# Kernel tuning notes

Hardware: AMD Instinct MI355X
Metric: run time of the kernel (lower is better)

Reference implementation:

```python
import jax, jax.numpy as jnp
import numpy as np

B_SZ, SEQ, CH, ORDER = 8, 8192, 256, 64
EPS_LN = 1e-5
EPS_H = 1e-6


def setup_inputs() -> dict:
    key = jax.random.key(0)
    ks = jax.random.split(key, 12)
    s = 1.0 / np.sqrt(CH)
    x = jax.random.normal(ks[0], (B_SZ, SEQ, CH), jnp.float32)
    # RTF params: A = denominator coeffs (monic, leading 1 implied), B = numerator coeffs
    A = 0.01 * jax.random.normal(ks[1], (CH, ORDER), jnp.float32)  # small -> stable 1/A(z)
    Bp = 0.1 * jax.random.normal(ks[2], (CH, ORDER), jnp.float32)
    h0 = jnp.zeros((1,), jnp.float32)  # init torch.tensor([0.])
    W_enc = s * jax.random.normal(ks[3], (CH, CH), jnp.float32)
    b_enc = jnp.zeros((CH,), jnp.float32)
    W_fc = s * jax.random.normal(ks[4], (CH, CH), jnp.float32)
    b_fc = jnp.zeros((CH,), jnp.float32)
    gamma = jnp.ones((CH,), jnp.float32)
    beta = jnp.zeros((CH,), jnp.float32)
    W_dec = s * jax.random.normal(ks[5], (CH, CH), jnp.float32)
    b_dec = jnp.zeros((CH,), jnp.float32)
    return {"x": x, "A": A, "Bp": Bp, "h0": h0, "W_enc": W_enc, "b_enc": b_enc,
            "W_fc": W_fc, "b_fc": b_fc, "gamma": gamma, "beta": beta,
            "W_dec": W_dec, "b_dec": b_dec}


def _rtf_kernel(A, Bp, L):
    # K(z) = B(z)/A(z) with monic denominator a = [1, A_1..A_order]
    C = A.shape[0]
    a = jnp.concatenate([jnp.ones((C, 1), A.dtype), A], axis=1)  # (C, order+1)
    af = jnp.fft.rfft(a, n=L, axis=1)
    bf = jnp.fft.rfft(Bp, n=L, axis=1)
    return jnp.fft.irfft(bf / af, n=L, axis=1)  # (C, L)


def _causal_fft_conv(x, K):
    # x: (B, L, C); K: (C, L) per-channel causal filter
    L = x.shape[1]
    n = 2 * L
    xf = jnp.fft.rfft(x, n=n, axis=1)            # (B, n/2+1, C)
    Kf = jnp.fft.rfft(K.T, n=n, axis=0)          # (n/2+1, C)
    return jnp.fft.irfft(xf * Kf[None], n=n, axis=1)[:, :L]


def reference(x, A, Bp, h0, W_enc, b_enc, W_fc, b_fc, gamma, beta, W_dec, b_dec):
    gelu = lambda t: jax.nn.gelu(t, approximate=False)
    xe = x @ W_enc.T + b_enc                      # encode
    L = xe.shape[1]
    K = _rtf_kernel(A, Bp, L)                     # kernel generation from (A,B)
    h1 = _causal_fft_conv(xe, K)                  # FFT long convolution
    y1 = gelu(h1 + h0 * xe)                       # SSMRTF output (mult_activation=gelu)
    y2 = gelu(y1 @ W_fc.T + b_fc)                 # fc + final_act
    y2 = y2 + xe                                  # skip
    mu = jnp.mean(y2, axis=-1, keepdims=True)     # LayerNorm over channels
    var = jnp.mean(jnp.square(y2 - mu), axis=-1, keepdims=True)
    y2 = (y2 - mu) * jax.lax.rsqrt(var + EPS_LN) * gamma + beta
    y = y2 @ W_dec.T + b_dec                      # decode
    # h = ||y||_inf over seq / ||x_enc||_inf over seq
    h = jnp.max(jnp.abs(y), axis=1) / (jnp.max(jnp.abs(xe), axis=1) + EPS_H)
    return (y, h)
```

## Files before the change

kernel.cpp:

```cpp
#include <hip/hip_runtime.h>
#include <math.h>


#define BSZ   8
#define SEQ   8192
#define CHN   256
#define ORD   64
#define STAPS 512
#define NDD   17
#define PREPAD 544
#define XROW  (PREPAD + SEQ)
#define MTOT  (BSZ * SEQ)
#define YELEMS (MTOT * CHN)

#define CT     2048
#define CROWE  3072

typedef short s16x8 __attribute__((ext_vector_type(8)));
typedef float f32x4 __attribute__((ext_vector_type(4)));

#define MFMA16(a, b, c) __builtin_amdgcn_mfma_f32_16x16x32_bf16((a), (b), (c), 0, 0, 0)

__device__ __forceinline__ void gll16(const void* g, void* l) {
  __builtin_amdgcn_global_load_lds(
      (const __attribute__((address_space(1))) unsigned int*)g,
      (__attribute__((address_space(3))) unsigned int*)l, 16, 0, 0);
}

#define PERMC(row, h) (((row) * 8 + ((h) ^ ((row) & 7))) * 8)

__device__ __forceinline__ unsigned short f2bf(float f) {
  unsigned u = __float_as_uint(f);
  return (unsigned short)((u + 0x7FFFu + ((u >> 16) & 1u)) >> 16);
}
__device__ __forceinline__ float bf2f(unsigned short h) {
  return __uint_as_float(((unsigned)h) << 16);
}
__device__ __forceinline__ float geluf(float x) {
  float x2 = x * x;
  float y = x * __builtin_fmaf(0.0356774081f, x2, 0.7978845608f);
  float e = __builtin_amdgcn_exp2f(-2.8853900818f * y);
  return x * __builtin_amdgcn_rcpf(1.0f + e);
}
__device__ __forceinline__ uint4 packbf8(float4 a, float4 b) {
  uint4 r;
  r.x = (unsigned)f2bf(a.x) | ((unsigned)f2bf(a.y) << 16);
  r.y = (unsigned)f2bf(a.z) | ((unsigned)f2bf(a.w) << 16);
  r.z = (unsigned)f2bf(b.x) | ((unsigned)f2bf(b.y) << 16);
  r.w = (unsigned)f2bf(b.z) | ((unsigned)f2bf(b.w) << 16);
  return r;
}

__global__ __launch_bounds__(256) void k_prep(const float* we, const float* wf,
                                              const float* wd, unsigned short* owe,
                                              unsigned short* owf, unsigned short* owd) {
  int i = blockIdx.x * 256 + threadIdx.x;
  int which = i >> 16, off = i & 65535;
  if (which == 0)      owe[off] = f2bf(we[off]);
  else if (which == 1) owf[off] = f2bf(wf[off]);
  else                 owd[off] = f2bf(wd[off]);
}

__global__ __launch_bounds__(256) void k_zero(unsigned short* xeT, uint4* maxbufs) {
  int i = blockIdx.x * 256 + threadIdx.x;
  uint4 z; z.x = 0; z.y = 0; z.z = 0; z.w = 0;
  if (i < 2048 * 68) {
    int row = i / 68, cc = i % 68;
    *(uint4*)((char*)xeT + (size_t)row * (XROW * 2) + (size_t)cc * 16) = z;
  } else {
    int j = i - 2048 * 68;
    if (j < 1024) maxbufs[j] = z;
  }
}

__global__ __launch_bounds__(256) void k_kgen(const float* A, const float* Bp,
                                              unsigned short* afr) {
  __shared__ float Gs[4][STAPS];
  __shared__ float Et[4][64];
  __shared__ float Ac[4][65];
  __shared__ float Bb[4][64];
  __shared__ float Kb[4][STAPS];
  int lane = threadIdx.x & 63, wv = threadIdx.x >> 6;
  int c = blockIdx.x * 4 + wv;
  Ac[wv][lane + 1] = A[(size_t)c * ORD + lane];
  Bb[wv][lane]     = Bp[(size_t)c * ORD + lane];
  if (lane == 0) { Ac[wv][0] = 1.f; Gs[wv][0] = 1.f; }
  __syncthreads();

  for (int n = 1; n < STAPS; n <<= 1) {
    float e = 0.f;
    int uhi = min(n + lane, 64);
    for (int u = lane + 1; u <= uhi; ++u)
      e += Ac[wv][u] * Gs[wv][n + lane - u];
    Et[wv][lane] = e;
    __syncthreads();
    int nk = (n + 63) >> 6;
    for (int k = 0; k < nk; ++k) {
      int idx = k * 64 + lane;
      if (idx < n) {
        float acc = 0.f;
        int imax = min(idx, 63);
        for (int i = 0; i <= imax; ++i)
          acc += Et[wv][i] * Gs[wv][idx - i];
        Gs[wv][n + idx] = -acc;
      }
    }
    __syncthreads();
  }

  for (int k = 0; k < 8; ++k) {
    int t = k * 64 + lane;
    float acc = 0.f;
    int jmax = min(t, 63);
    for (int j = 0; j <= jmax; ++j)
      acc += Bb[wv][j] * Gs[wv][t - j];
    Kb[wv][t] = acc;
  }
  __syncthreads();

  int m = lane & 15, quad = lane >> 4;
  for (int dd = 0; dd < NDD; ++dd) {
    unsigned short v[8];
#pragma unroll
    for (int j = 0; j < 8; ++j) {
      int k = quad * 8 + j;
      int d = 2 * dd + (k >> 4);
      int p = k & 15;
      int s = 16 * d + m - p;
      float kv = (s >= 0 && s < STAPS) ? Kb[wv][s] : 0.f;
      v[j] = f2bf(kv);
    }
    uint4 pk;
    pk.x = (unsigned)v[0] | ((unsigned)v[1] << 16);
    pk.y = (unsigned)v[2] | ((unsigned)v[3] << 16);
    pk.z = (unsigned)v[4] | ((unsigned)v[5] << 16);
    pk.w = (unsigned)v[6] | ((unsigned)v[7] << 16);
    *(uint4*)(afr + ((size_t)(c * NDD + dd) * 64 + lane) * 8) = pk;
  }
}

__global__ __launch_bounds__(256) void k_gemm1(const float* x, const unsigned short* wb,
                                               const float* benc, unsigned short* xeT,
                                               unsigned int* maxxe) {
  __shared__ __align__(16) unsigned short As[256 * 64];
  __shared__ __align__(16) unsigned short Bs[64 * 64];
  int tid = threadIdx.x, lane = tid & 63, wv = tid >> 6;
  int ln15 = lane & 15, hf = lane >> 4;
  size_t t0 = (size_t)blockIdx.x * 64;
  int b = (int)(t0 >> 13), tin = (int)(t0 & 8191);
  f32x4 acc[4][4];
#pragma unroll
  for (int i = 0; i < 4; ++i)
#pragma unroll
    for (int j = 0; j < 4; ++j) { acc[i][j][0]=0.f; acc[i][j][1]=0.f; acc[i][j][2]=0.f; acc[i][j][3]=0.f; }

  for (int k0 = 0; k0 < CHN; k0 += 64) {
    __syncthreads();
#pragma unroll
    for (int i = 0; i < 8; ++i) {
      int p = 512 * wv + 64 * i + lane;
      int row = p >> 3, h = (p & 7) ^ (row & 7);
      gll16(wb + (size_t)row * CHN + k0 + h * 8, &As[(512 * wv + 64 * i) * 8]);
    }
    {
      int row = tid >> 2, hb = (tid & 3) * 2;
      const float* src = x + (t0 + row) * CHN + k0 + hb * 8;
      float4 f0 = *(const float4*)src;
      float4 f1 = *(const float4*)(src + 4);
      float4 f2 = *(const float4*)(src + 8);
      float4 f3 = *(const float4*)(src + 12);
      *(uint4*)&Bs[PERMC(row, hb)]     = packbf8(f0, f1);
      *(uint4*)&Bs[PERMC(row, hb + 1)] = packbf8(f2, f3);
    }
    __syncthreads();
#pragma unroll
    for (int ks = 0; ks < 2; ++ks) {
      s16x8 af[4], bfr[4];
#pragma unroll
      for (int mt = 0; mt < 4; ++mt) {
        int row = 64 * wv + 16 * mt + ln15;
        af[mt] = *(const s16x8*)&As[PERMC(row, ks * 4 + hf)];
      }
#pragma unroll
      for (int nt = 0; nt < 4; ++nt) {
        int row = 16 * nt + ln15;
        bfr[nt] = *(const s16x8*)&Bs[PERMC(row, ks * 4 + hf)];
      }
#pragma unroll
      for (int mt = 0; mt < 4; ++mt)
#pragma unroll
        for (int nt = 0; nt < 4; ++nt)
          acc[mt][nt] = MFMA16(af[mt], bfr[nt], acc[mt][nt]);
    }
  }
  int quad = hf;
#pragma unroll
  for (int mt = 0; mt < 4; ++mt) {
#pragma unroll
    for (int r = 0; r < 4; ++r) {
      int row = 64 * wv + 16 * mt + 4 * quad + r;
      float bias = benc[row];
      float mv = 0.f;
#pragma unroll
      for (int nt = 0; nt < 4; ++nt) {
        float v = acc[mt][nt][r] + bias;
        int t = tin + 16 * nt + ln15;
        xeT[(size_t)(b * CHN + row) * XROW + PREPAD + t] = f2bf(v);
        mv = fmaxf(mv, fabsf(v));
      }
      mv = fmaxf(mv, __shfl_xor(mv, 1)); mv = fmaxf(mv, __shfl_xor(mv, 2));
      mv = fmaxf(mv, __shfl_xor(mv, 4)); mv = fmaxf(mv, __shfl_xor(mv, 8));
      if (ln15 == 0) atomicMax(&maxxe[b * CHN + row], __float_as_uint(mv));
    }
  }
}

__global__ __launch_bounds__(256) void k_conv(const unsigned short* xeT,
                                              const unsigned short* afr,
                                              unsigned short* y1, const float* h0p) {
  __shared__ __align__(16) unsigned short xet[4 * CROWE];
  __shared__ __align__(16) unsigned short bnc[4 * CT];
  int tid = threadIdx.x, lane = tid & 63, wv = tid >> 6;
  int idx = blockIdx.x;
  int tg = idx & 3, cg = (idx >> 2) & 63, b = idx >> 8;
  int c0 = cg * 4, t0 = tg * CT;
  int c = c0 + wv;

  s16x8 afrg[NDD];
  {
    const unsigned short* ap = afr + (size_t)c * (NDD * 512) + (size_t)lane * 8;
#pragma unroll
    for (int dd = 0; dd < NDD; ++dd)
      afrg[dd] = *(const s16x8*)(ap + (size_t)dd * 512);
  }
  {
    int lp = lane ^ ((lane >> 3) & 7);
    const unsigned short* gbase = xeT + (size_t)(b * CHN + c) * XROW + t0;
    unsigned short* lbase = &xet[wv * CROWE];
#pragma unroll
    for (int k = 0; k < 6; ++k)
      gll16(gbase + (size_t)(64 * k + lp) * 8, &lbase[k * 64 * 8]);
  }
  float h0 = h0p[0];

  int n = lane & 15, quad = lane >> 4;
  int qc = quad - ((quad >> 1) << 2);
  const char* xb = (const char*)&xet[wv * CROWE];

  int ad[NDD];
  {
    int cb0 = 2 * n + qc + 68;
#pragma unroll
    for (int dd = 0; dd < NDD; ++dd) {
      int cc = cb0 - 4 * dd;
      ad[dd] = (cc ^ ((cc >> 3) & 7)) * 16;
    }
  }
  int ead;
  {
    int ch = 68 + 2 * n + (quad >> 1);
    ead = (ch ^ ((ch >> 3) & 7)) * 16 + 8 * (quad & 1);
  }
  __syncthreads();

#pragma unroll 1
  for (int s = 0; s < 8; ++s) {
    f32x4 a0, a1;
    a0[0]=0.f; a0[1]=0.f; a0[2]=0.f; a0[3]=0.f;
    a1[0]=0.f; a1[1]=0.f; a1[2]=0.f; a1[3]=0.f;
#pragma unroll
    for (int dd = 0; dd < 16; dd += 2) {
      a0 = MFMA16(afrg[dd],     *(const s16x8*)(xb + ad[dd]),     a0);
      a1 = MFMA16(afrg[dd + 1], *(const s16x8*)(xb + ad[dd + 1]), a1);
    }
    a0 = MFMA16(afrg[16], *(const s16x8*)(xb + ad[16]), a0);
    uint2 xvp = *(const uint2*)(xb + ead);
    unsigned short o[4];
#pragma unroll
    for (int r = 0; r < 4; ++r) {
      float xv = bf2f(((const unsigned short*)&xvp)[r]);
      float v = (a0[r] + a1[r]) + h0 * xv;
      o[r] = f2bf(geluf(v));
    }
    uint2 pw;
    pw.x = (unsigned)o[0] | ((unsigned)o[1] << 16);
    pw.y = (unsigned)o[2] | ((unsigned)o[3] << 16);
    *(uint2*)&bnc[wv * CT + 256 * s + 16 * n + 4 * quad] = pw;
#pragma unroll
    for (int dd = 16; dd >= 8; --dd) ad[dd] = ad[dd - 8];
#pragma unroll
    for (int dd = 0; dd < 8; ++dd) ad[dd] = (ad[dd] + 512) ^ 64;
    ead = (ead + 512) ^ 64;
  }
  __syncthreads();
  {
    const size_t obase = (size_t)(b * SEQ + t0) * CHN + c0;
#pragma unroll
    for (int s = 0; s < 8; ++s) {
      int tl = 256 * s + tid;
      uint2 pk;
      pk.x = (unsigned)bnc[tl] | ((unsigned)bnc[CT + tl] << 16);
      pk.y = (unsigned)bnc[2 * CT + tl] | ((unsigned)bnc[3 * CT + tl] << 16);
      *(uint2*)(y1 + obase + (size_t)tl * CHN) = pk;
    }
  }
}

__global__ __launch_bounds__(256) void k_gemm2(const unsigned short* y1,
                                               const unsigned short* wb, const float* bfc,
                                               const unsigned short* xeT, const float* gam,
                                               const float* bet, unsigned short* y2n) {
  __shared__ __align__(16) unsigned short Ws[256 * 64];
  __shared__ __align__(16) unsigned short Asb[64 * 64];
  __shared__ float pl[64][2][2];
  int tid = threadIdx.x, lane = tid & 63, wv = tid >> 6;
  int ln15 = lane & 15, hf = lane >> 4, quad = hf;
  size_t M0 = (size_t)blockIdx.x * 64;
  int b = (int)(M0 >> 13), tin = (int)(M0 & 8191);
  int mh = wv & 1, nh = wv >> 1;
  f32x4 acc[2][8];
#pragma unroll
  for (int i = 0; i < 2; ++i)
#pragma unroll
    for (int j = 0; j < 8; ++j) { acc[i][j][0]=0.f; acc[i][j][1]=0.f; acc[i][j][2]=0.f; acc[i][j][3]=0.f; }

  for (int k0 = 0; k0 < CHN; k0 += 64) {
    __syncthreads();
#pragma unroll
    for (int i = 0; i < 8; ++i) {
      int p = 512 * wv + 64 * i + lane;
      int row = p >> 3, h = (p & 7) ^ (row & 7);
      gll16(wb + (size_t)row * CHN + k0 + h * 8, &Ws[(512 * wv + 64 * i) * 8]);
    }
#pragma unroll
    for (int i = 0; i < 2; ++i) {
      int p = 128 * wv + 64 * i + lane;
      int row = p >> 3, h = (p & 7) ^ (row & 7);
      gll16(y1 + (M0 + row) * CHN + k0 + h * 8, &Asb[(128 * wv + 64 * i) * 8]);
    }
    __syncthreads();
#pragma unroll
    for (int ks = 0; ks < 2; ++ks) {
      s16x8 af[2], bfr[8];
#pragma unroll
      for (int mt = 0; mt < 2; ++mt) {
        int row = 32 * mh + 16 * mt + ln15;
        af[mt] = *(const s16x8*)&Asb[PERMC(row, ks * 4 + hf)];
      }
#pragma unroll
      for (int nt = 0; nt < 8; ++nt) {
        int row = 128 * nh + 16 * nt + ln15;
        bfr[nt] = *(const s16x8*)&Ws[PERMC(row, ks * 4 + hf)];
      }
#pragma unroll
      for (int mt = 0; mt < 2; ++mt)
#pragma unroll
        for (int nt = 0; nt < 8; ++nt)
          acc[mt][nt] = MFMA16(af[mt], bfr[nt], acc[mt][nt]);
    }
  }
  float g8[8], be8[8], bf8[8];
#pragma unroll
  for (int nt = 0; nt < 8; ++nt) {
    int col = 128 * nh + 16 * nt + ln15;
    g8[nt] = gam[col]; be8[nt] = bet[col]; bf8[nt] = bfc[col];
  }
#pragma unroll
  for (int mt = 0; mt < 2; ++mt) {
    int mlb = 32 * mh + 16 * mt + 4 * quad;
    uint2 xv2[8];
#pragma unroll
    for (int nt = 0; nt < 8; ++nt) {
      int col = 128 * nh + 16 * nt + ln15;
      xv2[nt] = *(const uint2*)(xeT + (size_t)(b * CHN + col) * XROW + PREPAD + tin + mlb);
    }
#pragma unroll
    for (int r = 0; r < 4; ++r) {
      int ml = mlb + r;
      float s1 = 0.f, s2 = 0.f;
#pragma unroll
      for (int nt = 0; nt < 8; ++nt) {
        float t2 = acc[mt][nt][r] + bf8[nt];
        float xv = bf2f(((const unsigned short*)&xv2[nt])[r]);
        float y2 = geluf(t2) + xv;
        acc[mt][nt][r] = y2;
        s1 += y2; s2 += y2 * y2;
      }
      s1 += __shfl_xor(s1, 1); s2 += __shfl_xor(s2, 1);
      s1 += __shfl_xor(s1, 2); s2 += __shfl_xor(s2, 2);
      s1 += __shfl_xor(s1, 4); s2 += __shfl_xor(s2, 4);
      s1 += __shfl_xor(s1, 8); s2 += __shfl_xor(s2, 8);
      if (ln15 == 0) { pl[ml][nh][0] = s1; pl[ml][nh][1] = s2; }
    }
  }
  __syncthreads();
#pragma unroll
  for (int mt = 0; mt < 2; ++mt) {
#pragma unroll
    for (int r = 0; r < 4; ++r) {
      int ml = 32 * mh + 16 * mt + 4 * quad + r;
      float s1 = pl[ml][0][0] + pl[ml][1][0];
      float s2 = pl[ml][0][1] + pl[ml][1][1];
      float mu = s1 * (1.f / 256.f);
      float var = s2 * (1.f / 256.f) - mu * mu;
      float ri = rsqrtf(var + 1e-5f);
#pragma unroll
      for (int nt = 0; nt < 8; ++nt) {
        int col = 128 * nh + 16 * nt + ln15;
        float yn = (acc[mt][nt][r] - mu) * ri * g8[nt] + be8[nt];
        y2n[(M0 + ml) * CHN + col] = f2bf(yn);
      }
    }
  }
}

__global__ __launch_bounds__(256) void k_gemm3(const unsigned short* y2n,
                                               const unsigned short* wb, const float* bd,
                                               float* yout, unsigned int* maxy) {
  __shared__ __align__(16) unsigned short Ws[256 * 64];
  __shared__ __align__(16) unsigned short Asb[64 * 64];
  int tid = threadIdx.x, lane = tid & 63, wv = tid >> 6;
  int ln15 = lane & 15, hf = lane >> 4, quad = hf;
  size_t M0 = (size_t)blockIdx.x * 64;
  int b = (int)(M0 >> 13);
  int mh = wv & 1, nh = wv >> 1;
  f32x4 acc[2][8];
#pragma unroll
  for (int i = 0; i < 2; ++i)
#pragma unroll
    for (int j = 0; j < 8; ++j) { acc[i][j][0]=0.f; acc[i][j][1]=0.f; acc[i][j][2]=0.f; acc[i][j][3]=0.f; }

  for (int k0 = 0; k0 < CHN; k0 += 64) {
    __syncthreads();
#pragma unroll
    for (int i = 0; i < 8; ++i) {
      int p = 512 * wv + 64 * i + lane;
      int row = p >> 3, h = (p & 7) ^ (row & 7);
      gll16(wb + (size_t)row * CHN + k0 + h * 8, &Ws[(512 * wv + 64 * i) * 8]);
    }
#pragma unroll
    for (int i = 0; i < 2; ++i) {
      int p = 128 * wv + 64 * i + lane;
      int row = p >> 3, h = (p & 7) ^ (row & 7);
      gll16(y2n + (M0 + row) * CHN + k0 + h * 8, &Asb[(128 * wv + 64 * i) * 8]);
    }
    __syncthreads();
#pragma unroll
    for (int ks = 0; ks < 2; ++ks) {
      s16x8 af[2], bfr[8];
#pragma unroll
      for (int mt = 0; mt < 2; ++mt) {
        int row = 32 * mh + 16 * mt + ln15;
        af[mt] = *(const s16x8*)&Asb[PERMC(row, ks * 4 + hf)];
      }
#pragma unroll
      for (int nt = 0; nt < 8; ++nt) {
        int row = 128 * nh + 16 * nt + ln15;
        bfr[nt] = *(const s16x8*)&Ws[PERMC(row, ks * 4 + hf)];
      }
#pragma unroll
      for (int mt = 0; mt < 2; ++mt)
#pragma unroll
        for (int nt = 0; nt < 8; ++nt)
          acc[mt][nt] = MFMA16(af[mt], bfr[nt], acc[mt][nt]);
    }
  }
  float bd8[8];
#pragma unroll
  for (int nt = 0; nt < 8; ++nt) bd8[nt] = bd[128 * nh + 16 * nt + ln15];
#pragma unroll
  for (int mt = 0; mt < 2; ++mt)
#pragma unroll
    for (int r = 0; r < 4; ++r) {
      int ml = 32 * mh + 16 * mt + 4 * quad + r;
#pragma unroll
      for (int nt = 0; nt < 8; ++nt) {
        int col = 128 * nh + 16 * nt + ln15;
        float v = acc[mt][nt][r] + bd8[nt];
        acc[mt][nt][r] = v;
        yout[(M0 + ml) * CHN + col] = v;
      }
    }
#pragma unroll
  for (int nt = 0; nt < 8; ++nt) {
    int col = 128 * nh + 16 * nt + ln15;
    float mv = 0.f;
#pragma unroll
    for (int mt = 0; mt < 2; ++mt)
#pragma unroll
      for (int r = 0; r < 4; ++r) mv = fmaxf(mv, fabsf(acc[mt][nt][r]));
    mv = fmaxf(mv, __shfl_xor(mv, 16));
    mv = fmaxf(mv, __shfl_xor(mv, 32));
    if (quad == 0) atomicMax(&maxy[b * CHN + col], __float_as_uint(mv));
  }
}

__global__ __launch_bounds__(256) void k_hfin(const unsigned int* maxxe,
                                              const unsigned int* maxy, float* hout) {
  int i = blockIdx.x * 256 + threadIdx.x;
  if (i < BSZ * CHN) {
    float mx = __uint_as_float(maxxe[i]);
    float my = __uint_as_float(maxy[i]);
    hout[i] = my / (mx + 1e-6f);
  }
}

extern "C" void kernel_launch(void* const* d_in, const int* in_sizes, int n_in,
                              void* d_out, int out_size, void* d_ws, size_t ws_size,
                              hipStream_t stream) {
  const float* x   = (const float*)d_in[0];
  const float* A   = (const float*)d_in[1];
  const float* Bp  = (const float*)d_in[2];
  const float* h0  = (const float*)d_in[3];
  const float* We  = (const float*)d_in[4];
  const float* be  = (const float*)d_in[5];
  const float* Wf  = (const float*)d_in[6];
  const float* bfc = (const float*)d_in[7];
  const float* gam = (const float*)d_in[8];
  const float* bet = (const float*)d_in[9];
  const float* Wd  = (const float*)d_in[10];
  const float* bd  = (const float*)d_in[11];

  char* ws = (char*)d_ws;
  unsigned short* y1  = (unsigned short*)(ws + 0);
  unsigned short* afr = (unsigned short*)(ws + 33554432);
  unsigned short* web = (unsigned short*)(ws + 38010880);
  unsigned short* wfb = (unsigned short*)(ws + 38141952);
  unsigned short* wdb = (unsigned short*)(ws + 38273024);
  unsigned int*  maxxe = (unsigned int*)(ws + 38404096);
  unsigned int*  maxy  = (unsigned int*)(ws + 38412288);

  unsigned short* xeT = (unsigned short*)d_out;
  float* yout = (float*)d_out;
  float* hout = yout + YELEMS;

  k_prep<<<768, 256, 0, stream>>>(We, Wf, Wd, web, wfb, wdb);
  k_zero<<<548, 256, 0, stream>>>(xeT, (uint4*)maxxe);
  k_kgen<<<64, 256, 0, stream>>>(A, Bp, afr);
  k_gemm1<<<1024, 256, 0, stream>>>(x, web, be, xeT, maxxe);
  k_conv<<<2048, 256, 0, stream>>>(xeT, afr, y1, h0);
  k_gemm2<<<1024, 256, 0, stream>>>(y1, wfb, bfc, xeT, gam, bet, y1);
  k_gemm3<<<1024, 256, 0, stream>>>(y1, wdb, bd, yout, maxy);
  k_hfin<<<8, 256, 0, stream>>>(maxxe, maxy, hout);
}
```

Baseline: 296.8 us.

## Merge prep/zero kernels and fold kernel generation into first GEMM launch

Combines weight conversion and buffer zeroing into one launch, and runs the RTF kernel-generation work as 64 extra blocks inside the encoder GEMM launch so the two overlap. The kgen code now keeps the A coefficients in registers and uses fully unrolled fixed-length loops over a zero-padded shared buffer, replacing the variable-bound loops. This removes two launch boundaries and the serial latency of the small kgen kernel, at the cost of more registers and shared memory in the combined GEMM kernel, which may lower its occupancy.

Measured after the change: 279.6 us. -5.8%, faster.

```diff
diff --git a/kernel.cpp b/kernel.cpp
--- a/kernel.cpp
+++ b/kernel.cpp
@@ -51,59 +51,66 @@
   return r;
 }
 
-__global__ __launch_bounds__(256) void k_prep(const float* we, const float* wf,
-                                              const float* wd, unsigned short* owe,
-                                              unsigned short* owf, unsigned short* owd) {
-  int i = blockIdx.x * 256 + threadIdx.x;
-  int which = i >> 16, off = i & 65535;
-  if (which == 0)      owe[off] = f2bf(we[off]);
-  else if (which == 1) owf[off] = f2bf(wf[off]);
-  else                 owd[off] = f2bf(wd[off]);
-}
-
-__global__ __launch_bounds__(256) void k_zero(unsigned short* xeT, uint4* maxbufs) {
-  int i = blockIdx.x * 256 + threadIdx.x;
-  uint4 z; z.x = 0; z.y = 0; z.z = 0; z.w = 0;
-  if (i < 2048 * 68) {
-    int row = i / 68, cc = i % 68;
-    *(uint4*)((char*)xeT + (size_t)row * (XROW * 2) + (size_t)cc * 16) = z;
+__global__ __launch_bounds__(256) void k_pz(const float* we, const float* wf,
+                                            const float* wd, unsigned short* owe,
+                                            unsigned short* owf, unsigned short* owd,
+                                            unsigned short* xeT, uint4* maxbufs) {
+  int bx = blockIdx.x, tid = threadIdx.x;
+  if (bx < 768) {
+    int i = bx * 256 + tid;
+    int which = i >> 16, off = i & 65535;
+    if (which == 0)      owe[off] = f2bf(we[off]);
+    else if (which == 1) owf[off] = f2bf(wf[off]);
+    else                 owd[off] = f2bf(wd[off]);
   } else {
-    int j = i - 2048 * 68;
-    if (j < 1024) maxbufs[j] = z;
-  }
-}
-
-__global__ __launch_bounds__(256) void k_kgen(const float* A, const float* Bp,
-                                              unsigned short* afr) {
-  __shared__ float Gs[4][STAPS];
-  __shared__ float Et[4][64];
-  __shared__ float Ac[4][65];
-  __shared__ float Bb[4][64];
-  __shared__ float Kb[4][STAPS];
-  int lane = threadIdx.x & 63, wv = threadIdx.x >> 6;
-  int c = blockIdx.x * 4 + wv;
-  Ac[wv][lane + 1] = A[(size_t)c * ORD + lane];
-  Bb[wv][lane]     = Bp[(size_t)c * ORD + lane];
-  if (lane == 0) { Ac[wv][0] = 1.f; Gs[wv][0] = 1.f; }
+    int i = (bx - 768) * 256 + tid;
+    uint4 z; z.x = 0; z.y = 0; z.z = 0; z.w = 0;
+    if (i < 2048 * 68) {
+      int row = i / 68, cc = i % 68;
+      *(uint4*)((char*)xeT + (size_t)row * (XROW * 2) + (size_t)cc * 16) = z;
+    } else {
+      int j = i - 2048 * 68;
+      if (j < 1024) maxbufs[j] = z;
+    }
+  }
+}
+
+__device__ __forceinline__ void kgen_body(char* smem, const float* A, const float* Bp,
+                                          unsigned short* afr, int blk) {
+  int tid = threadIdx.x, lane = tid & 63;
+  int wv = __builtin_amdgcn_readfirstlane(tid >> 6);
+  int c = blk * 4 + wv;
+  float* base = (float*)smem + wv * 1152;
+  float* Gsp = base;
+  float* Et  = base + 576;
+  float* Kb  = base + 640;
+  const float* Ap = A + (size_t)c * ORD;
+  const float* Bb = Bp + (size_t)c * ORD;
+
+  float Au[64];
+#pragma unroll
+  for (int u = 0; u < 64; ++u) Au[u] = Ap[u];
+
+#pragma unroll
+  for (int k = 0; k < 9; ++k) Gsp[k * 64 + lane] = 0.f;
+  if (lane == 0) Gsp[64] = 1.f;
   __syncthreads();
 
   for (int n = 1; n < STAPS; n <<= 1) {
     float e = 0.f;
-    int uhi = min(n + lane, 64);
-    for (int u = lane + 1; u <= uhi; ++u)
-      e += Ac[wv][u] * Gs[wv][n + lane - u];
-    Et[wv][lane] = e;
+#pragma unroll
+    for (int u = 1; u <= 64; ++u)
+      e += Au[u - 1] * Gsp[64 + n + lane - u];
+    Et[lane] = e;
     __syncthreads();
     int nk = (n + 63) >> 6;
     for (int k = 0; k < nk; ++k) {
       int idx = k * 64 + lane;
-      if (idx < n) {
-        float acc = 0.f;
-        int imax = min(idx, 63);
-        for (int i = 0; i <= imax; ++i)
-          acc += Et[wv][i] * Gs[wv][idx - i];
-        Gs[wv][n + idx] = -acc;
-      }
+      float acc = 0.f;
+#pragma unroll
+      for (int i = 0; i < 64; ++i)
+        acc += Et[i] * Gsp[64 + idx - i];
+      if (idx < n) Gsp[64 + n + idx] = -acc;
     }
     __syncthreads();
   }
@@ -111,10 +118,10 @@
   for (int k = 0; k < 8; ++k) {
     int t = k * 64 + lane;
     float acc = 0.f;
-    int jmax = min(t, 63);
-    for (int j = 0; j <= jmax; ++j)
-      acc += Bb[wv][j] * Gs[wv][t - j];
-    Kb[wv][t] = acc;
+#pragma unroll
+    for (int j = 0; j < 64; ++j)
+      acc += Bb[j] * Gsp[64 + t - j];
+    Kb[t] = acc;
   }
   __syncthreads();
 
@@ -127,7 +134,7 @@
       int d = 2 * dd + (k >> 4);
       int p = k & 15;
       int s = 16 * d + m - p;
-      float kv = (s >= 0 && s < STAPS) ? Kb[wv][s] : 0.f;
+      float kv = (s >= 0 && s < STAPS) ? Kb[s] : 0.f;
       v[j] = f2bf(kv);
     }
     uint4 pk;
@@ -139,14 +146,21 @@
   }
 }
 
-__global__ __launch_bounds__(256) void k_gemm1(const float* x, const unsigned short* wb,
-                                               const float* benc, unsigned short* xeT,
-                                               unsigned int* maxxe) {
-  __shared__ __align__(16) unsigned short As[256 * 64];
-  __shared__ __align__(16) unsigned short Bs[64 * 64];
+__global__ __launch_bounds__(256) void k_g1k(const float* A, const float* Bp,
+                                             unsigned short* afr,
+                                             const float* x, const unsigned short* wb,
+                                             const float* benc, unsigned short* xeT,
+                                             unsigned int* maxxe) {
+  __shared__ __align__(16) char smem[40960];
+  if (blockIdx.x < 64) {
+    kgen_body(smem, A, Bp, afr, blockIdx.x);
+    return;
+  }
+  unsigned short* As = (unsigned short*)smem;
+  unsigned short* Bs = (unsigned short*)(smem + 32768);
   int tid = threadIdx.x, lane = tid & 63, wv = tid >> 6;
   int ln15 = lane & 15, hf = lane >> 4;
-  size_t t0 = (size_t)blockIdx.x * 64;
+  size_t t0 = (size_t)(blockIdx.x - 64) * 64;
   int b = (int)(t0 >> 13), tin = (int)(t0 & 8191);
   f32x4 acc[4][4];
 #pragma unroll
@@ -534,10 +548,8 @@
   float* yout = (float*)d_out;
   float* hout = yout + YELEMS;
 
-  k_prep<<<768, 256, 0, stream>>>(We, Wf, Wd, web, wfb, wdb);
-  k_zero<<<548, 256, 0, stream>>>(xeT, (uint4*)maxxe);
-  k_kgen<<<64, 256, 0, stream>>>(A, Bp, afr);
-  k_gemm1<<<1024, 256, 0, stream>>>(x, web, be, xeT, maxxe);
+  k_pz<<<1316, 256, 0, stream>>>(We, Wf, Wd, web, wfb, wdb, xeT, (uint4*)maxxe);
+  k_g1k<<<1088, 256, 0, stream>>>(A, Bp, afr, x, web, be, xeT, maxxe);
   k_conv<<<2048, 256, 0, stream>>>(xeT, afr, y1, h0);
   k_gemm2<<<1024, 256, 0, stream>>>(y1, wfb, bfc, xeT, gam, bet, y1);
   k_gemm3<<<1024, 256, 0, stream>>>(y1, wdb, bd, yout, maxy);
```
